# Optimization experiments

Hardware: AMD Instinct MI355X
Metric: run time of the kernel (lower is better)

Reference implementation:

```python
import jax, jax.numpy as jnp
import numpy as np

HEADS = 8
WINDOW = 16

def _pointwise(W, b, t):
    # Conv1d(C, C, kernel=1): (B, C, T) -> (B, C, T)
    return jnp.einsum('oc,bct->bot', W, t) + b[None, :, None]

def setup_inputs() -> dict:
    key = jax.random.key(0)
    ks = jax.random.split(key, 10)
    B, C, T = 4, 512, 4096
    s = 0.02
    return {
        'x':    jax.random.normal(ks[0], (B, C, T), jnp.float32),
        'cond': jax.random.normal(ks[1], (B, C, T), jnp.float32),
        'Wq': jax.random.normal(ks[2], (C, C), jnp.float32) * s,
        'bq': jnp.zeros((C,), jnp.float32),
        'Wk': jax.random.normal(ks[3], (C, C), jnp.float32) * s,
        'bk': jnp.zeros((C,), jnp.float32),
        'Wv': jax.random.normal(ks[4], (C, C), jnp.float32) * s,
        'bv': jnp.zeros((C,), jnp.float32),
        'Wo': jax.random.normal(ks[5], (C, C), jnp.float32) * s,
        'bo': jnp.zeros((C,), jnp.float32),
    }

def reference(x, cond, Wq, bq, Wk, bk, Wv, bv, Wo, bo):
    B, C, T = x.shape
    H, W = HEADS, WINDOW
    hd = C // H
    scale = hd ** (-0.5)
    pad_left = W // 2          # 8
    pad_right = W - pad_left - 1  # 7

    q = _pointwise(Wq, bq, x)      # (B, C, T)
    k = _pointwise(Wk, bk, cond)
    v = _pointwise(Wv, bv, cond)

    k = jnp.pad(k, ((0, 0), (0, 0), (pad_left, pad_right)))  # (B, C, T+W-1)
    v = jnp.pad(v, ((0, 0), (0, 0), (pad_left, pad_right)))

    # sliding windows of size W, stride 1 -> T_unf == T
    idx = jnp.arange(T)[:, None] + jnp.arange(W)[None, :]  # (T, W)
    k_win = k[:, :, idx].reshape(B, H, hd, T, W)
    v_win = v[:, :, idx].reshape(B, H, hd, T, W)
    qh = q.reshape(B, H, hd, T)

    dots = jnp.einsum('bhdt,bhdtw->bhtw', qh, k_win) * scale
    attn = jax.nn.softmax(dots, axis=-1)
    out = jnp.einsum('bhtw,bhdtw->bhdt', attn, v_win)  # (B, H, hd, T)
    out = out.reshape(B, C, T)
    return _pointwise(Wo, bo, out)
```

## Files before the change

### kernel.cpp

```cpp
#include <hip/hip_runtime.h>

#define CC 512
#define TT 4096
#define NB 4
#define NH 8
#define HD 64

typedef __attribute__((ext_vector_type(8))) short s16x8;
typedef __attribute__((ext_vector_type(4))) float f32x4;
typedef __attribute__((ext_vector_type(4))) unsigned int u32x4;

#if defined(__has_builtin)
#  if __has_builtin(__builtin_amdgcn_fdot2_f32_bf16)
#    define HAS_BF16_DOT2 1
#  else
#    define HAS_BF16_DOT2 0
#  endif
#else
#  define HAS_BF16_DOT2 0
#endif

__device__ __forceinline__ short f2bf(float f) {
    unsigned u = __float_as_uint(f);
    unsigned r = (u + 0x7fffu + ((u >> 16) & 1u)) >> 16;
    return (short)r;
}
__device__ __forceinline__ float bf2f(short s) {
    return __uint_as_float(((unsigned)(unsigned short)s) << 16);
}

#if HAS_BF16_DOT2
typedef __attribute__((ext_vector_type(2))) __bf16 bf16x2;
__device__ __forceinline__ float dot2bf(unsigned a, unsigned b, float c) {
    return __builtin_amdgcn_fdot2_f32_bf16(__builtin_bit_cast(bf16x2, a),
                                           __builtin_bit_cast(bf16x2, b), c, false);
}
#else
__device__ __forceinline__ float dot2bf(unsigned a, unsigned b, float c) {
    float r = fmaf(bf2f((short)(a & 0xffffu)), bf2f((short)(b & 0xffffu)), c);
    return fmaf(bf2f((short)(a >> 16)), bf2f((short)(b >> 16)), r);
}
#endif

__device__ __forceinline__ void gld_lds16(const void* g, void* s) {
    __builtin_amdgcn_global_load_lds(
        (const __attribute__((address_space(1))) unsigned int*)g,
        (__attribute__((address_space(3))) unsigned int*)s, 16, 0, 0);
}

__global__ __launch_bounds__(256) void cvt_w_k(const float* __restrict__ w0,
                                               const float* __restrict__ w1,
                                               const float* __restrict__ w2,
                                               const float* __restrict__ w3,
                                               short* __restrict__ dst) {
    int i = blockIdx.x * 256 + threadIdx.x;
    const float* s = (i < 262144) ? w0 : (i < 524288) ? w1 : (i < 786432) ? w2 : w3;
    dst[i] = f2bf(s[i & 262143]);
}

__global__ __launch_bounds__(256) void trans_k(const float* __restrict__ x,
                                               const float* __restrict__ cond,
                                               short* __restrict__ xT,
                                               short* __restrict__ condT) {
    __shared__ float tile[64][65];
    int z = blockIdx.z;
    int b = z & 3;
    const float* src = (z < 4 ? x : cond) + (size_t)b * CC * TT;
    short* dst = (z < 4 ? xT : condT) + (size_t)b * TT * CC;
    int tx = threadIdx.x & 63, ty = threadIdx.x >> 6;
    int t0 = blockIdx.x * 64, c0 = blockIdx.y * 64;
#pragma unroll
    for (int r = 0; r < 64; r += 4)
        tile[ty + r][tx] = src[(size_t)(c0 + ty + r) * TT + t0 + tx];
    __syncthreads();
#pragma unroll
    for (int r = 0; r < 64; r += 4)
        dst[(size_t)(t0 + ty + r) * CC + c0 + tx] = f2bf(tile[tx][ty + r]);
}

template <int TMAJOR>
__device__ __forceinline__ void gemm128(const short* __restrict__ Wm,
                                        const short* __restrict__ Sm,
                                        const float* __restrict__ bias,
                                        float* __restrict__ Df,
                                        short* __restrict__ Db) {
    __shared__ short Al[128 * 64] __attribute__((aligned(16)));
    __shared__ short Bl[128 * 64] __attribute__((aligned(16)));
    const int tid = threadIdx.x;
    const int lane = tid & 63;
    const int wid = tid >> 6;
    const int o0 = blockIdx.y * 128;
    const int t0 = blockIdx.x * 128;
    const int wm = (wid >> 1) * 64;
    const int wn = (wid & 1) * 64;

    f32x4 acc[4][4];
#pragma unroll
    for (int i = 0; i < 4; i++)
#pragma unroll
        for (int j = 0; j < 4; j++) acc[i][j] = (f32x4){0.f, 0.f, 0.f, 0.f};

    const int cbase = (wid * 4) << 6;

    for (int kt = 0; kt < 8; ++kt) {
        const int k0 = kt * 64;
        __syncthreads();
#pragma unroll
        for (int j = 0; j < 4; ++j) {
            int c = cbase + (j << 6) + lane;
            int m = c >> 3, kc = c & 7;
            int kcs = kc ^ (m & 7);
            gld_lds16(Wm + (size_t)(o0 + m) * CC + k0 + kcs * 8,
                      &Al[(cbase + (j << 6)) << 3]);
            gld_lds16(Sm + (size_t)(t0 + m) * CC + k0 + kcs * 8,
                      &Bl[(cbase + (j << 6)) << 3]);
        }
        __syncthreads();
#pragma unroll
        for (int kk = 0; kk < 2; ++kk) {
            const int kb = kk * 32 + (lane >> 4) * 8;
            s16x8 af[4], bfr[4];
#pragma unroll
            for (int i = 0; i < 4; i++) {
                int m = wm + i * 16 + (lane & 15);
                af[i] = *(const s16x8*)&Al[(m * 64 + kb) ^ ((m & 7) << 3)];
                int n = wn + i * 16 + (lane & 15);
                bfr[i] = *(const s16x8*)&Bl[(n * 64 + kb) ^ ((n & 7) << 3)];
            }
#pragma unroll
            for (int mi = 0; mi < 4; mi++)
#pragma unroll
                for (int ni = 0; ni < 4; ni++) {
                    if (TMAJOR)
                        acc[mi][ni] = __builtin_amdgcn_mfma_f32_16x16x32_bf16(
                            bfr[mi], af[ni], acc[mi][ni], 0, 0, 0);
                    else
                        acc[mi][ni] = __builtin_amdgcn_mfma_f32_16x16x32_bf16(
                            af[mi], bfr[ni], acc[mi][ni], 0, 0, 0);
                }
        }
    }

    const int col = lane & 15;
    const int rg = (lane >> 4) << 2;
    if (TMAJOR) {
#pragma unroll
        for (int ti = 0; ti < 4; ti++) {
            int t = t0 + wn + ti * 16 + rg;
#pragma unroll
            for (int oi = 0; oi < 4; oi++) {
                int o = o0 + wm + oi * 16 + col;
                float bv = bias[o];
                f32x4 a = acc[ti][oi];
#pragma unroll
                for (int r = 0; r < 4; r++)
                    Db[(size_t)(t + r) * CC + o] = f2bf(a[r] + bv);
            }
        }
    } else {
#pragma unroll
        for (int mi = 0; mi < 4; mi++) {
            int o = o0 + wm + mi * 16 + rg;
#pragma unroll
            for (int ni = 0; ni < 4; ni++) {
                int t = t0 + wn + ni * 16 + col;
                f32x4 a = acc[mi][ni];
#pragma unroll
                for (int r = 0; r < 4; r++)
                    Df[(size_t)(o + r) * TT + t] = a[r] + bias[o + r];
            }
        }
    }
}

__global__ __launch_bounds__(256, 2) void gemm_qkv_k(
    const short* __restrict__ Wb, const short* __restrict__ xT,
    const short* __restrict__ condT, const float* __restrict__ bq,
    const float* __restrict__ bk, const float* __restrict__ bv,
    short* __restrict__ qkvT) {
    int z = blockIdx.z, which = z >> 2, b = z & 3;
    const short* Wm = Wb + (size_t)which * CC * CC;
    const short* Sm = (which == 0 ? xT : condT) + (size_t)b * TT * CC;
    const float* bias = which == 0 ? bq : (which == 1 ? bk : bv);
    short* Db = qkvT + ((size_t)which * NB + b) * TT * CC;
    gemm128<1>(Wm, Sm, bias, nullptr, Db);
}

__global__ __launch_bounds__(256, 2) void gemm_o_k(const short* __restrict__ Wb,
                                                   const short* __restrict__ outT,
                                                   const float* __restrict__ bo,
                                                   float* __restrict__ out) {
    int b = blockIdx.z;
    gemm128<0>(Wb + 3 * (size_t)CC * CC, outT + (size_t)b * TT * CC, bo,
               out + (size_t)b * CC * TT, nullptr);
}

__global__ __launch_bounds__(64) void attn3_k(const short* __restrict__ qkvT,
                                              short* __restrict__ outT) {
    __shared__ unsigned kl[640 * 4] __attribute__((aligned(16)));
    __shared__ unsigned vl[640 * 4] __attribute__((aligned(16)));
    const int lane = threadIdx.x;
    const int t0 = blockIdx.x * 64;
    const int h = blockIdx.y, b = blockIdx.z;
    const size_t BTC = (size_t)NB * TT * CC;
    const short* qg = qkvT + (size_t)b * TT * CC + h * HD;
    const short* kg = qg + BTC;
    const short* vg = qg + 2 * BTC;

    u32x4 qv[8];
    {
        const u32x4* qr = (const u32x4*)(qg + (size_t)(t0 + lane) * CC);
#pragma unroll
        for (int c = 0; c < 8; ++c) qv[c] = qr[c];
    }

#pragma unroll
    for (int it = 0; it < 10; ++it) {
        int idx = it * 64 + lane;
        int row = idx >> 3, s = idx & 7;
        int c = s ^ (row & 7);
        int t = t0 - 8 + row;
        u32x4 kv = {0u, 0u, 0u, 0u};
        u32x4 vv = {0u, 0u, 0u, 0u};
        if ((unsigned)t < (unsigned)TT) {
            kv = *(const u32x4*)&kg[(size_t)t * CC + c * 8];
            vv = *(const u32x4*)&vg[(size_t)t * CC + c * 8];
        }
        *(u32x4*)&kl[idx * 4] = kv;
        *(u32x4*)&vl[idx * 4] = vv;
    }
    __syncthreads();

    float dots[16];
#pragma unroll
    for (int w = 0; w < 16; ++w) {
        const int row = lane + w;
        float acc = 0.f;
#pragma unroll
        for (int c = 0; c < 8; ++c) {
            u32x4 kc = *(const u32x4*)&kl[(row * 8 + (c ^ (row & 7))) * 4];
#pragma unroll
            for (int d = 0; d < 4; ++d) acc = dot2bf(qv[c][d], kc[d], acc);
        }
        dots[w] = acc * 0.125f;
    }

    float mx = dots[0];
#pragma unroll
    for (int w = 1; w < 16; ++w) mx = fmaxf(mx, dots[w]);
    float e[16], sum = 0.f;
#pragma unroll
    for (int w = 0; w < 16; ++w) {
        e[w] = __expf(dots[w] - mx);
        sum += e[w];
    }
    const float inv = 1.f / sum;

    unsigned pp[8];
#pragma unroll
    for (int i = 0; i < 8; ++i)
        pp[i] = (unsigned)(unsigned short)f2bf(e[2 * i] * inv) |
                ((unsigned)(unsigned short)f2bf(e[2 * i + 1] * inv) << 16);

    float of[64];
#pragma unroll
    for (int j = 0; j < 64; ++j) of[j] = 0.f;
#pragma unroll
    for (int i = 0; i < 8; ++i) {
        const int r0 = lane + 2 * i, r1 = r0 + 1;
#pragma unroll
        for (int c = 0; c < 8; ++c) {
            u32x4 va = *(const u32x4*)&vl[(r0 * 8 + (c ^ (r0 & 7))) * 4];
            u32x4 vb = *(const u32x4*)&vl[(r1 * 8 + (c ^ (r1 & 7))) * 4];
#pragma unroll
            for (int d = 0; d < 4; ++d) {
                unsigned lo = __builtin_amdgcn_perm(vb[d], va[d], 0x05040100u);
                unsigned hi = __builtin_amdgcn_perm(vb[d], va[d], 0x07060302u);
                of[c * 8 + 2 * d]     = dot2bf(pp[i], lo, of[c * 8 + 2 * d]);
                of[c * 8 + 2 * d + 1] = dot2bf(pp[i], hi, of[c * 8 + 2 * d + 1]);
            }
        }
    }

    short* ob = outT + ((size_t)b * TT + t0 + lane) * CC + h * HD;
#pragma unroll
    for (int c = 0; c < 8; ++c) {
        s16x8 pk;
#pragma unroll
        for (int j = 0; j < 8; ++j) pk[j] = f2bf(of[c * 8 + j]);
        *(s16x8*)&ob[c * 8] = pk;
    }
}

extern "C" void kernel_launch(void* const* d_in, const int* in_sizes, int n_in,
                              void* d_out, int out_size, void* d_ws, size_t ws_size,
                              hipStream_t stream) {
    const float* x    = (const float*)d_in[0];
    const float* cond = (const float*)d_in[1];
    const float* Wq   = (const float*)d_in[2];
    const float* bq   = (const float*)d_in[3];
    const float* Wk   = (const float*)d_in[4];
    const float* bk   = (const float*)d_in[5];
    const float* Wv   = (const float*)d_in[6];
    const float* bv   = (const float*)d_in[7];
    const float* Wo   = (const float*)d_in[8];
    const float* bo   = (const float*)d_in[9];

    char* ws = (char*)d_ws;
    short* Wb    = (short*)ws;
    short* xT    = (short*)(ws + (2u << 20));
    short* condT = (short*)(ws + (18u << 20));
    short* qkvT  = (short*)(ws + (34u << 20));
    short* outT  = xT;

    cvt_w_k<<<4096, 256, 0, stream>>>(Wq, Wk, Wv, Wo, Wb);
    trans_k<<<dim3(TT / 64, CC / 64, 8), 256, 0, stream>>>(x, cond, xT, condT);
    gemm_qkv_k<<<dim3(TT / 128, CC / 128, 12), 256, 0, stream>>>(Wb, xT, condT, bq, bk, bv, qkvT);
    attn3_k<<<dim3(TT / 64, NH, NB), 64, 0, stream>>>(qkvT, outT);
    gemm_o_k<<<dim3(TT / 128, CC / 128, 4), 256, 0, stream>>>(Wb, outT, bo, (float*)d_out);
}
```

Before: 94.13 us.

## Share one LDS band for K then V with direct global-to-LDS loads

The attention kernel now uses a single shared-memory band instead of separate K and V buffers. K is loaded with direct global-to-LDS copies, the dots are computed, and then V is streamed into the same buffer while softmax runs. Boundary rows are clamped instead of zero-filled and masked explicitly, and the output accumulation is split into two halves to reduce register pressure, with a launch bound of 4 blocks. This aims to halve LDS use, raise occupancy and overlap the V load with softmax compute. In exchange it adds a second barrier and a hand-written waitcnt.

```diff
diff --git a/kernel.cpp b/kernel.cpp
--- a/kernel.cpp
+++ b/kernel.cpp
@@ -195,10 +195,9 @@
                out + (size_t)b * CC * TT, nullptr);
 }
 
-__global__ __launch_bounds__(64) void attn3_k(const short* __restrict__ qkvT,
-                                              short* __restrict__ outT) {
-    __shared__ unsigned kl[640 * 4] __attribute__((aligned(16)));
-    __shared__ unsigned vl[640 * 4] __attribute__((aligned(16)));
+__global__ __launch_bounds__(64, 4) void attn4_k(const short* __restrict__ qkvT,
+                                                 short* __restrict__ outT) {
+    __shared__ unsigned band[640 * 4] __attribute__((aligned(16)));
     const int lane = threadIdx.x;
     const int t0 = blockIdx.x * 64;
     const int h = blockIdx.y, b = blockIdx.z;
@@ -207,88 +206,106 @@
     const short* kg = qg + BTC;
     const short* vg = qg + 2 * BTC;
 
-    u32x4 qv[8];
-    {
-        const u32x4* qr = (const u32x4*)(qg + (size_t)(t0 + lane) * CC);
-#pragma unroll
-        for (int c = 0; c < 8; ++c) qv[c] = qr[c];
-    }
-
 #pragma unroll
     for (int it = 0; it < 10; ++it) {
         int idx = it * 64 + lane;
         int row = idx >> 3, s = idx & 7;
         int c = s ^ (row & 7);
         int t = t0 - 8 + row;
-        u32x4 kv = {0u, 0u, 0u, 0u};
-        u32x4 vv = {0u, 0u, 0u, 0u};
-        if ((unsigned)t < (unsigned)TT) {
-            kv = *(const u32x4*)&kg[(size_t)t * CC + c * 8];
-            vv = *(const u32x4*)&vg[(size_t)t * CC + c * 8];
-        }
-        *(u32x4*)&kl[idx * 4] = kv;
-        *(u32x4*)&vl[idx * 4] = vv;
-    }
+        t = t < 0 ? 0 : (t > TT - 1 ? TT - 1 : t);
+        gld_lds16(kg + (size_t)t * CC + c * 8, &band[it * 256]);
+    }
+
+    float dots[16];
+    {
+        u32x4 qv[8];
+        const u32x4* qr = (const u32x4*)(qg + (size_t)(t0 + lane) * CC);
+#pragma unroll
+        for (int c = 0; c < 8; ++c) qv[c] = qr[c];
+
+        __syncthreads();
+
+#pragma unroll
+        for (int w = 0; w < 16; ++w) {
+            const int row = lane + w;
+            float acc = 0.f;
+#pragma unroll
+            for (int c = 0; c < 8; ++c) {
+                u32x4 kc = *(const u32x4*)&band[(row * 8 + (c ^ (row & 7))) * 4];
+#pragma unroll
+                for (int d = 0; d < 4; ++d) acc = dot2bf(qv[c][d], kc[d], acc);
+            }
+            int s = t0 - 8 + row;
+            dots[w] = ((unsigned)s < (unsigned)TT) ? acc * 0.125f : 0.f;
+        }
+    }
+
+    asm volatile("s_waitcnt lgkmcnt(0)" ::: "memory");
+
+#pragma unroll
+    for (int it = 0; it < 10; ++it) {
+        int idx = it * 64 + lane;
+        int row = idx >> 3, s = idx & 7;
+        int c = s ^ (row & 7);
+        int t = t0 - 8 + row;
+        t = t < 0 ? 0 : (t > TT - 1 ? TT - 1 : t);
+        gld_lds16(vg + (size_t)t * CC + c * 8, &band[it * 256]);
+    }
+
+    unsigned pp[8];
+    {
+        float mx = dots[0];
+#pragma unroll
+        for (int w = 1; w < 16; ++w) mx = fmaxf(mx, dots[w]);
+        float e[16], sum = 0.f;
+#pragma unroll
+        for (int w = 0; w < 16; ++w) {
+            e[w] = __expf(dots[w] - mx);
+            sum += e[w];
+        }
+        const float inv = 1.f / sum;
+        const int sb = t0 - 8 + lane;
+#pragma unroll
+        for (int i = 0; i < 8; ++i) {
+            float p0 = ((unsigned)(sb + 2 * i) < (unsigned)TT) ? e[2 * i] * inv : 0.f;
+            float p1 = ((unsigned)(sb + 2 * i + 1) < (unsigned)TT) ? e[2 * i + 1] * inv : 0.f;
+            pp[i] = (unsigned)(unsigned short)f2bf(p0) |
+                    ((unsigned)(unsigned short)f2bf(p1) << 16);
+        }
+    }
+
     __syncthreads();
 
-    float dots[16];
-#pragma unroll
-    for (int w = 0; w < 16; ++w) {
-        const int row = lane + w;
-        float acc = 0.f;
-#pragma unroll
-        for (int c = 0; c < 8; ++c) {
-            u32x4 kc = *(const u32x4*)&kl[(row * 8 + (c ^ (row & 7))) * 4];
-#pragma unroll
-            for (int d = 0; d < 4; ++d) acc = dot2bf(qv[c][d], kc[d], acc);
-        }
-        dots[w] = acc * 0.125f;
-    }
-
-    float mx = dots[0];
-#pragma unroll
-    for (int w = 1; w < 16; ++w) mx = fmaxf(mx, dots[w]);
-    float e[16], sum = 0.f;
-#pragma unroll
-    for (int w = 0; w < 16; ++w) {
-        e[w] = __expf(dots[w] - mx);
-        sum += e[w];
-    }
-    const float inv = 1.f / sum;
-
-    unsigned pp[8];
-#pragma unroll
-    for (int i = 0; i < 8; ++i)
-        pp[i] = (unsigned)(unsigned short)f2bf(e[2 * i] * inv) |
-                ((unsigned)(unsigned short)f2bf(e[2 * i + 1] * inv) << 16);
-
-    float of[64];
-#pragma unroll
-    for (int j = 0; j < 64; ++j) of[j] = 0.f;
-#pragma unroll
-    for (int i = 0; i < 8; ++i) {
-        const int r0 = lane + 2 * i, r1 = r0 + 1;
-#pragma unroll
-        for (int c = 0; c < 8; ++c) {
-            u32x4 va = *(const u32x4*)&vl[(r0 * 8 + (c ^ (r0 & 7))) * 4];
-            u32x4 vb = *(const u32x4*)&vl[(r1 * 8 + (c ^ (r1 & 7))) * 4];
-#pragma unroll
-            for (int d = 0; d < 4; ++d) {
-                unsigned lo = __builtin_amdgcn_perm(vb[d], va[d], 0x05040100u);
-                unsigned hi = __builtin_amdgcn_perm(vb[d], va[d], 0x07060302u);
-                of[c * 8 + 2 * d]     = dot2bf(pp[i], lo, of[c * 8 + 2 * d]);
-                of[c * 8 + 2 * d + 1] = dot2bf(pp[i], hi, of[c * 8 + 2 * d + 1]);
-            }
-        }
-    }
-
     short* ob = outT + ((size_t)b * TT + t0 + lane) * CC + h * HD;
 #pragma unroll
-    for (int c = 0; c < 8; ++c) {
-        s16x8 pk;
-#pragma unroll
-        for (int j = 0; j < 8; ++j) pk[j] = f2bf(of[c * 8 + j]);
-        *(s16x8*)&ob[c * 8] = pk;
+    for (int half = 0; half < 2; ++half) {
+        float of[32];
+#pragma unroll
+        for (int j = 0; j < 32; ++j) of[j] = 0.f;
+#pragma unroll
+        for (int i = 0; i < 8; ++i) {
+            const int r0 = lane + 2 * i, r1 = r0 + 1;
+#pragma unroll
+            for (int cl = 0; cl < 4; ++cl) {
+                const int c = half * 4 + cl;
+                u32x4 va = *(const u32x4*)&band[(r0 * 8 + (c ^ (r0 & 7))) * 4];
+                u32x4 vb = *(const u32x4*)&band[(r1 * 8 + (c ^ (r1 & 7))) * 4];
+#pragma unroll
+                for (int d = 0; d < 4; ++d) {
+                    unsigned lo = __builtin_amdgcn_perm(vb[d], va[d], 0x05040100u);
+                    unsigned hi = __builtin_amdgcn_perm(vb[d], va[d], 0x07060302u);
+                    of[cl * 8 + 2 * d]     = dot2bf(pp[i], lo, of[cl * 8 + 2 * d]);
+                    of[cl * 8 + 2 * d + 1] = dot2bf(pp[i], hi, of[cl * 8 + 2 * d + 1]);
+                }
+            }
+        }
+#pragma unroll
+        for (int cl = 0; cl < 4; ++cl) {
+            s16x8 pk;
+#pragma unroll
+            for (int j = 0; j < 8; ++j) pk[j] = f2bf(of[cl * 8 + j]);
+            *(s16x8*)&ob[half * 32 + cl * 8] = pk;
+        }
     }
 }
 
@@ -316,6 +333,6 @@
     cvt_w_k<<<4096, 256, 0, stream>>>(Wq, Wk, Wv, Wo, Wb);
     trans_k<<<dim3(TT / 64, CC / 64, 8), 256, 0, stream>>>(x, cond, xT, condT);
     gemm_qkv_k<<<dim3(TT / 128, CC / 128, 12), 256, 0, stream>>>(Wb, xT, condT, bq, bk, bv, qkvT);
-    attn3_k<<<dim3(TT / 64, NH, NB), 64, 0, stream>>>(qkvT, outT);
+    attn4_k<<<dim3(TT / 64, NH, NB), 64, 0, stream>>>(qkvT, outT);
     gemm_o_k<<<dim3(TT / 128, CC / 128, 4), 256, 0, stream>>>(Wb, outT, bo, (float*)d_out);
 }
```

New measurement: 108.1 us. 1.15x slower.
